# Kernel tuning notes

Measured on AMD Instinct MI355X. Metric: run time of the kernel, lower is better.

The kernel has to match this reference:

```python
import jax, jax.numpy as jnp
import numpy as np

N_NODES = 100000
N_EDGES = 1600000


def gcn_conv(h_in, row, col, W, b, num_nodes):
    """PyG-style GCNConv: linear transform, add self-loops, symmetric
    deg^{-1/2} normalization, scatter-add aggregation at target nodes."""
    h = h_in @ W  # [N, out]
    loops = jnp.arange(num_nodes, dtype=row.dtype)
    r = jnp.concatenate([row, loops])  # source
    c = jnp.concatenate([col, loops])  # target
    ew = jnp.ones(r.shape[0], dtype=h.dtype)
    deg = jax.ops.segment_sum(ew, c, num_segments=num_nodes)  # in-degree incl. self-loop
    dinv = jnp.where(deg > 0, jax.lax.rsqrt(deg), 0.0)
    norm = dinv[r] * dinv[c]  # [E+N]
    msgs = norm[:, None] * h[r]  # gather + scale, [E+N, out]
    out = jax.ops.segment_sum(msgs, c, num_segments=num_nodes)  # scatter-add
    return out + b


def setup_inputs() -> dict:
    key = jax.random.key(0)
    ks = jax.random.split(key, 8)
    in_f, hid, out_f = 128, 128, 64
    x = jax.random.normal(ks[0], (N_NODES, in_f), dtype=jnp.float32)
    edge_index = jax.random.randint(ks[1], (2, N_EDGES), 0, N_NODES, dtype=jnp.int64)
    edge_weight = jax.random.uniform(ks[2], (N_EDGES,), dtype=jnp.float32)
    s1 = 1.0 / np.sqrt(in_f)
    s2 = 1.0 / np.sqrt(hid)
    s3 = 1.0 / np.sqrt(out_f)
    W1 = jax.random.normal(ks[3], (in_f, hid), dtype=jnp.float32) * s1
    b1 = jnp.zeros((hid,), dtype=jnp.float32)
    W2 = jax.random.normal(ks[4], (hid, out_f), dtype=jnp.float32) * s2
    b2 = jnp.zeros((out_f,), dtype=jnp.float32)
    Wfc = jax.random.normal(ks[5], (out_f, 1), dtype=jnp.float32) * s3
    bfc = jnp.zeros((1,), dtype=jnp.float32)
    return {"x": x, "edge_index": edge_index, "edge_weight": edge_weight,
            "W1": W1, "b1": b1, "W2": W2, "b2": b2, "Wfc": Wfc, "bfc": bfc}


def reference(x, edge_index, edge_weight, W1, b1, W2, b2, Wfc, bfc):
    # eval mode: dropout(p=0.6) is identity; edge_weight is unused by the
    # original forward (edge_attr never passed to GCNConv).
    row, col = edge_index[0], edge_index[1]
    n = x.shape[0]
    h = jax.nn.relu(gcn_conv(x, row, col, W1, b1, n))
    h = gcn_conv(h, row, col, W2, b2, n)
    return h @ Wfc + bfc  # [N, 1]
```

## Files before the change

### kernel.cpp

```cpp
#include <hip/hip_runtime.h>
#include <cstddef>

#define CAP 64
#define BK_SHIFT 8
#define BSTRIDE 8192
#define CHUNK 2048

typedef unsigned int uint32;
typedef unsigned short ushort;
typedef __attribute__((ext_vector_type(8))) short short8;
typedef __attribute__((ext_vector_type(4))) float f32x4;
typedef __attribute__((ext_vector_type(4))) int int4v;
typedef __attribute__((ext_vector_type(4))) float float4v;

__device__ __forceinline__ float bf_lo(uint32 v) {
  union { uint32 u; float f; } c; c.u = v << 16; return c.f;
}
__device__ __forceinline__ float bf_hi(uint32 v) {
  union { uint32 u; float f; } c; c.u = v & 0xffff0000u; return c.f;
}
__device__ __forceinline__ uint32 pack_bf2(float a, float b) {
  union { float f; uint32 u; } x, y; x.f = a; y.f = b;
  uint32 ua = x.u + 0x7fffu + ((x.u >> 16) & 1u);
  uint32 ub = y.u + 0x7fffu + ((y.u >> 16) & 1u);
  return (ua >> 16) | (ub & 0xffff0000u);
}
__device__ __forceinline__ ushort bf16_1(float x) {
  union { float f; uint32 u; } c; c.f = x;
  return (ushort)((c.u + 0x7fffu + ((c.u >> 16) & 1u)) >> 16);
}

union ABu { uint32 u[4]; short8 v; };

__global__ __launch_bounds__(256) void k_part1(const int* __restrict__ ei,
                                               int* __restrict__ bcnt,
                                               int* __restrict__ stage,
                                               int E, int N, int NB) {
  __shared__ int hist[512];
  __shared__ int gbase[512];
  const int tid = threadIdx.x;
  const int base = blockIdx.x * CHUNK;
  for (int b = tid; b < NB; b += 256) hist[b] = 0;
  __syncthreads();
  int rr[8], cc[8], lp[8];
  #pragma unroll
  for (int j = 0; j < 8; j++) {
    int e = base + tid + j * 256;
    int r = -1, c = -1;
    if (e < E) {
      r = __builtin_nontemporal_load(&ei[e]);
      c = __builtin_nontemporal_load(&ei[(size_t)E + e]);
    }
    bool ok = ((unsigned)r < (unsigned)N) && ((unsigned)c < (unsigned)N);
    rr[j] = ok ? r : -1;
    cc[j] = c;
    lp[j] = ok ? atomicAdd(&hist[c >> BK_SHIFT], 1) : 0;
  }
  __syncthreads();
  for (int b = tid; b < NB; b += 256) {
    int h = hist[b];
    gbase[b] = h ? atomicAdd(&bcnt[b], h) : 0;
  }
  __syncthreads();
  #pragma unroll
  for (int j = 0; j < 8; j++) {
    if (rr[j] >= 0) {
      int b = cc[j] >> BK_SHIFT;
      int pos = gbase[b] + lp[j];
      if (pos < BSTRIDE)
        stage[(size_t)b * BSTRIDE + pos] = (rr[j] << 8) | (cc[j] & 255);
    }
  }
}

__global__ __launch_bounds__(256) void k_fill2(const int* __restrict__ stage,
                                               const int* __restrict__ bcnt,
                                               int* __restrict__ csr,
                                               int* __restrict__ cnt,
                                               float* __restrict__ dinv, int N, int NB,
                                               const float* __restrict__ W2,
                                               const float* __restrict__ Wfc,
                                               const float* __restrict__ b2,
                                               const float* __restrict__ bfc,
                                               float* __restrict__ wvo,
                                               float* __restrict__ c0) {
  const int b = blockIdx.x;
  const int tid = threadIdx.x;
  if (b == NB) {
    if (tid < 128) {
      float s = 0.f;
      #pragma unroll 8
      for (int j = 0; j < 64; j++) s += W2[tid * 64 + j] * Wfc[j];
      wvo[tid] = s;
      if (tid == 0) {
        float cc = 0.f;
        for (int j = 0; j < 64; j++) cc += b2[j] * Wfc[j];
        c0[0] = cc + bfc[0];
      }
    }
    return;
  }
  __shared__ int lc[256];
  lc[tid] = 0;
  __syncthreads();
  int m = bcnt[b]; if (m > BSTRIDE) m = BSTRIDE;
  const int node0 = b << BK_SHIFT;
  const int* __restrict__ sb = stage + (size_t)b * BSTRIDE;
  for (int e = tid; e < m; e += 256) {
    int v = __builtin_nontemporal_load(&sb[e]);
    int cl = v & 255;
    int r = v >> 8;
    int pos = atomicAdd(&lc[cl], 1);
    if (pos < CAP) csr[(size_t)(node0 + cl) * CAP + pos] = r;
  }
  __syncthreads();
  int node = node0 + tid;
  if (node < N) {
    int d = lc[tid]; if (d > CAP) d = CAP;
    cnt[node] = d;
    int d8 = (d + 7) & ~7; if (d8 > CAP) d8 = CAP;
    for (int p = d; p < d8; p++) csr[(size_t)node * CAP + p] = node;
    dinv[node] = rsqrtf((float)(lc[tid] + 1));
  }
}

__global__ __launch_bounds__(256) void k_gemm(const float* __restrict__ X,
                                              const float* __restrict__ W,
                                              const float* __restrict__ dinv,
                                              ushort* __restrict__ Xh, int M) {
  __shared__ ushort WtT[16384];
  const int tid  = threadIdx.x;
  const int lane = tid & 63;
  const int wv   = tid >> 6;
  const int cl   = lane & 15;
  const int g    = lane >> 4;

  const int rb = blockIdx.x * 64 + wv * 16;

  int rowc = rb + cl; if (rowc >= M) rowc = M - 1;
  const float* xr = X + (size_t)rowc * 128;
  ABu af[4];
  #pragma unroll
  for (int kk = 0; kk < 4; kk++) {
    float4v p = __builtin_nontemporal_load((const float4v*)&xr[kk * 32 + g * 8]);
    float4v q = __builtin_nontemporal_load((const float4v*)&xr[kk * 32 + g * 8 + 4]);
    af[kk].u[0] = pack_bf2(p.x, p.y);
    af[kk].u[1] = pack_bf2(p.z, p.w);
    af[kk].u[2] = pack_bf2(q.x, q.y);
    af[kk].u[3] = pack_bf2(q.z, q.w);
  }

  float dvr[4];
  #pragma unroll
  for (int r = 0; r < 4; r++) {
    int rw = rb + g * 4 + r; if (rw >= M) rw = M - 1;
    dvr[r] = dinv[rw];
  }

  for (int idx = tid; idx < 8192; idx += 256) {
    int k = idx >> 6;
    int c = (idx & 63) * 2;
    float2 w2 = *(const float2*)&W[k * 128 + c];
    int gr = ((k >> 3) ^ ((c & 15) >> 1)) & 15;
    int base = (gr << 4) + (k & 7) * 2;
    *(ushort*)((char*)WtT + c * 256 + base)       = bf16_1(w2.x);
    *(ushort*)((char*)WtT + (c + 1) * 256 + base) = bf16_1(w2.y);
  }
  __syncthreads();

  #pragma unroll
  for (int ct = 0; ct < 8; ct++) {
    const char* wrow = (const char*)WtT + (ct * 16 + cl) * 256;
    f32x4 acc = {0.f, 0.f, 0.f, 0.f};
    #pragma unroll
    for (int kk = 0; kk < 4; kk++) {
      int grn = ((4 * kk + g) ^ (cl >> 1)) & 15;
      short8 bfrag = *(const short8*)(wrow + (grn << 4));
      acc = __builtin_amdgcn_mfma_f32_16x16x32_bf16(af[kk].v, bfrag, acc, 0, 0, 0);
    }
    #pragma unroll
    for (int r = 0; r < 4; r++) {
      int rw = rb + g * 4 + r;
      if (rw < M) Xh[(size_t)rw * 128 + ct * 16 + cl] = bf16_1(dvr[r] * acc[r]);
    }
  }
}

__global__ __launch_bounds__(256) void k_agg1(const uint32* __restrict__ Xh,
                                              const int* __restrict__ csr,
                                              const int* __restrict__ cnt,
                                              const float* __restrict__ dinv,
                                              const float* __restrict__ b1,
                                              const float* __restrict__ wv,
                                              float* __restrict__ dz, int N) {
  int wid = (blockIdx.x * 256 + threadIdx.x) >> 6;
  int lane = threadIdx.x & 63;
  if (wid >= N) return;
  const int i = wid;
  int deg = cnt[i]; if (deg > CAP) deg = CAP;
  const int deg8 = (deg + 7) & ~7;
  const float di = dinv[i];
  int edge_reg = i;
  if (lane < deg8) edge_reg = __builtin_nontemporal_load(&csr[(size_t)i * CAP + lane]);

  uint32 vs = Xh[(size_t)i * 64 + lane];
  float a0x = 0.f, a0y = 0.f, a1x = 0.f, a1y = 0.f;
  float a2x = 0.f, a2y = 0.f, a3x = 0.f, a3y = 0.f;
  float a4x = 0.f, a4y = 0.f, a5x = 0.f, a5y = 0.f;
  float a6x = 0.f, a6y = 0.f, a7x = 0.f, a7y = 0.f;

  for (int e = 0; e < deg8; e += 8) {
    int s0 = __builtin_amdgcn_readlane(edge_reg, e + 0);
    int s1 = __builtin_amdgcn_readlane(edge_reg, e + 1);
    int s2 = __builtin_amdgcn_readlane(edge_reg, e + 2);
    int s3 = __builtin_amdgcn_readlane(edge_reg, e + 3);
    int s4 = __builtin_amdgcn_readlane(edge_reg, e + 4);
    int s5 = __builtin_amdgcn_readlane(edge_reg, e + 5);
    int s6 = __builtin_amdgcn_readlane(edge_reg, e + 6);
    int s7 = __builtin_amdgcn_readlane(edge_reg, e + 7);
    uint32 v0 = Xh[(size_t)s0 * 64 + lane];
    uint32 v1 = Xh[(size_t)s1 * 64 + lane];
    uint32 v2 = Xh[(size_t)s2 * 64 + lane];
    uint32 v3 = Xh[(size_t)s3 * 64 + lane];
    uint32 v4 = Xh[(size_t)s4 * 64 + lane];
    uint32 v5 = Xh[(size_t)s5 * 64 + lane];
    uint32 v6 = Xh[(size_t)s6 * 64 + lane];
    uint32 v7 = Xh[(size_t)s7 * 64 + lane];
    a0x += bf_lo(v0); a0y += bf_hi(v0);
    a1x += bf_lo(v1); a1y += bf_hi(v1);
    a2x += bf_lo(v2); a2y += bf_hi(v2);
    a3x += bf_lo(v3); a3y += bf_hi(v3);
    a4x += bf_lo(v4); a4y += bf_hi(v4);
    a5x += bf_lo(v5); a5y += bf_hi(v5);
    a6x += bf_lo(v6); a6y += bf_hi(v6);
    a7x += bf_lo(v7); a7y += bf_hi(v7);
  }
  const float selfc = 1.0f - (float)(deg8 - deg);
  float sx = ((a0x + a1x) + (a2x + a3x)) + ((a4x + a5x) + (a6x + a7x));
  float sy = ((a0y + a1y) + (a2y + a3y)) + ((a4y + a5y) + (a6y + a7y));
  sx = fmaf(selfc, bf_lo(vs), sx);
  sy = fmaf(selfc, bf_hi(vs), sy);

  float2 bb = *(const float2*)&b1[lane * 2];
  float h0 = fmaxf(fmaf(di, sx, bb.x), 0.f);
  float h1 = fmaxf(fmaf(di, sy, bb.y), 0.f);
  float2 ww = *(const float2*)&wv[lane * 2];
  float part = fmaf(h0, ww.x, h1 * ww.y);
  #pragma unroll
  for (int m = 32; m > 0; m >>= 1) part += __shfl_xor(part, m, 64);
  if (lane == 0) dz[i] = di * part;
}

__global__ __launch_bounds__(256) void k_out(const float* __restrict__ dz,
                                             const int* __restrict__ csr,
                                             const int* __restrict__ cnt,
                                             const float* __restrict__ dinv,
                                             const float* __restrict__ c0,
                                             float* __restrict__ out, int N) {
  int i = blockIdx.x * 256 + threadIdx.x;
  if (i >= N) return;
  int deg = cnt[i]; if (deg > CAP) deg = CAP;
  const int deg8 = (deg + 7) & ~7;
  const int4v* __restrict__ edges = (const int4v*)(csr + (size_t)i * CAP);
  float s0 = (1.0f - (float)(deg8 - deg)) * dz[i];
  float s1 = 0.f, s2 = 0.f, s3 = 0.f;
  for (int e4 = 0; e4 < (deg8 >> 2); e4 += 2) {
    int4v q0 = __builtin_nontemporal_load(&edges[e4]);
    int4v q1 = __builtin_nontemporal_load(&edges[e4 + 1]);
    s0 += dz[q0.x]; s1 += dz[q0.y]; s2 += dz[q0.z]; s3 += dz[q0.w];
    s0 += dz[q1.x]; s1 += dz[q1.y]; s2 += dz[q1.z]; s3 += dz[q1.w];
  }
  out[i] = dinv[i] * ((s0 + s1) + (s2 + s3)) + c0[0];
}

extern "C" void kernel_launch(void* const* d_in, const int* in_sizes, int n_in,
                              void* d_out, int out_size, void* d_ws, size_t ws_size,
                              hipStream_t stream) {
  const float* x   = (const float*)d_in[0];
  const int*   ei  = (const int*)d_in[1];
  const float* W1  = (const float*)d_in[3];
  const float* b1  = (const float*)d_in[4];
  const float* W2  = (const float*)d_in[5];
  const float* b2  = (const float*)d_in[6];
  const float* Wfc = (const float*)d_in[7];
  const float* bfc = (const float*)d_in[8];
  float* out = (float*)d_out;

  const int N = in_sizes[0] / 128;
  const int E = in_sizes[1] / 2;
  const int NB = (N + 255) >> 8;

  char* ws = (char*)d_ws;
  ushort* Xh  = (ushort*)(ws);
  int*   stage= (int*)   (ws);
  int*   csr  = (int*)   (ws + (size_t)N * 256);
  int*   cnt  = (int*)   (ws + (size_t)N * 512);
  float* dinv = (float*) (ws + (size_t)N * 516);
  float* dz   = (float*) (ws + (size_t)N * 520);
  int*   bcnt = (int*)dz;
  float* wv   = (float*) (ws + (size_t)N * 524);
  float* c0   = wv + 128;

  hipMemsetAsync(bcnt, 0, (size_t)NB * 4, stream);
  hipLaunchKernelGGL(k_part1, dim3((E + CHUNK - 1) / CHUNK), dim3(256), 0, stream,
                     ei, bcnt, stage, E, N, NB);
  hipLaunchKernelGGL(k_fill2, dim3(NB + 1), dim3(256), 0, stream,
                     stage, bcnt, csr, cnt, dinv, N, NB, W2, Wfc, b2, bfc, wv, c0);
  hipLaunchKernelGGL(k_gemm,  dim3((N + 63) / 64), dim3(256), 0, stream,
                     x, W1, dinv, Xh, N);
  hipLaunchKernelGGL(k_agg1,  dim3(((size_t)N * 64 + 255) / 256), dim3(256), 0, stream,
                     (const uint32*)Xh, csr, cnt, dinv, b1, wv, dz, N);
  hipLaunchKernelGGL(k_out,   dim3((N + 255) / 256), dim3(256), 0, stream,
                     dz, csr, cnt, dinv, c0, out, N);
}
```

Baseline: 161.9 us.

## Slice hidden features into 16-wide planes and aggregate per slice with reduction

The GEMM output is stored as eight feature-sliced planes of 16 bf16 values per node. The first aggregation is rewritten so that each wave handles eight nodes, with eight lanes per node gathering 32-byte rows from a single slice. Partial dot products go to a per-slice buffer, and a new reduction kernel sums them into dz. The stored dinv array is dropped and rsqrt is recomputed from the degree counts, which adds a launch and extra partial-sum traffic in exchange for narrower, more parallel gathers.

```diff
diff --git a/kernel.cpp b/kernel.cpp
--- a/kernel.cpp
+++ b/kernel.cpp
@@ -76,8 +76,7 @@
 __global__ __launch_bounds__(256) void k_fill2(const int* __restrict__ stage,
                                                const int* __restrict__ bcnt,
                                                int* __restrict__ csr,
-                                               int* __restrict__ cnt,
-                                               float* __restrict__ dinv, int N, int NB,
+                                               int* __restrict__ cnt, int N, int NB,
                                                const float* __restrict__ W2,
                                                const float* __restrict__ Wfc,
                                                const float* __restrict__ b2,
@@ -120,22 +119,21 @@
     cnt[node] = d;
     int d8 = (d + 7) & ~7; if (d8 > CAP) d8 = CAP;
     for (int p = d; p < d8; p++) csr[(size_t)node * CAP + p] = node;
-    dinv[node] = rsqrtf((float)(lc[tid] + 1));
   }
 }
 
 __global__ __launch_bounds__(256) void k_gemm(const float* __restrict__ X,
                                               const float* __restrict__ W,
-                                              const float* __restrict__ dinv,
-                                              ushort* __restrict__ Xh, int M) {
+                                              const int* __restrict__ cnt,
+                                              ushort* __restrict__ Xh8, int M) {
   __shared__ ushort WtT[16384];
   const int tid  = threadIdx.x;
   const int lane = tid & 63;
   const int wv   = tid >> 6;
   const int cl   = lane & 15;
   const int g    = lane >> 4;
-
   const int rb = blockIdx.x * 64 + wv * 16;
+  const size_t SL = (size_t)M * 16;
 
   int rowc = rb + cl; if (rowc >= M) rowc = M - 1;
   const float* xr = X + (size_t)rowc * 128;
@@ -154,7 +152,7 @@
   #pragma unroll
   for (int r = 0; r < 4; r++) {
     int rw = rb + g * 4 + r; if (rw >= M) rw = M - 1;
-    dvr[r] = dinv[rw];
+    dvr[r] = rsqrtf((float)(cnt[rw] + 1));
   }
 
   for (int idx = tid; idx < 8192; idx += 256) {
@@ -181,80 +179,69 @@
     #pragma unroll
     for (int r = 0; r < 4; r++) {
       int rw = rb + g * 4 + r;
-      if (rw < M) Xh[(size_t)rw * 128 + ct * 16 + cl] = bf16_1(dvr[r] * acc[r]);
-    }
-  }
-}
-
-__global__ __launch_bounds__(256) void k_agg1(const uint32* __restrict__ Xh,
-                                              const int* __restrict__ csr,
-                                              const int* __restrict__ cnt,
-                                              const float* __restrict__ dinv,
-                                              const float* __restrict__ b1,
-                                              const float* __restrict__ wv,
-                                              float* __restrict__ dz, int N) {
-  int wid = (blockIdx.x * 256 + threadIdx.x) >> 6;
-  int lane = threadIdx.x & 63;
-  if (wid >= N) return;
-  const int i = wid;
+      if (rw < M) Xh8[(size_t)ct * SL + (size_t)rw * 16 + cl] = bf16_1(dvr[r] * acc[r]);
+    }
+  }
+}
+
+__global__ __launch_bounds__(256) void k_agg1s(const ushort* __restrict__ Xh8,
+                                               const int* __restrict__ csr,
+                                               const int* __restrict__ cnt,
+                                               const float* __restrict__ b1,
+                                               const float* __restrict__ wvv,
+                                               float* __restrict__ dzp, int M, int N) {
+  const int tid  = threadIdx.x;
+  const int s    = blockIdx.x & 7;
+  const int chnk = blockIdx.x >> 3;
+  const int lane = tid & 63;
+  const int ld   = lane & 7;
+  const int i    = chnk * 32 + (tid >> 6) * 8 + (lane >> 3);
+  if (i >= N) return;
+  const uint32* __restrict__ Xs = (const uint32*)(Xh8 + (size_t)s * (size_t)M * 16);
+
   int deg = cnt[i]; if (deg > CAP) deg = CAP;
   const int deg8 = (deg + 7) & ~7;
-  const float di = dinv[i];
-  int edge_reg = i;
-  if (lane < deg8) edge_reg = __builtin_nontemporal_load(&csr[(size_t)i * CAP + lane]);
-
-  uint32 vs = Xh[(size_t)i * 64 + lane];
-  float a0x = 0.f, a0y = 0.f, a1x = 0.f, a1y = 0.f;
-  float a2x = 0.f, a2y = 0.f, a3x = 0.f, a3y = 0.f;
-  float a4x = 0.f, a4y = 0.f, a5x = 0.f, a5y = 0.f;
-  float a6x = 0.f, a6y = 0.f, a7x = 0.f, a7y = 0.f;
-
-  for (int e = 0; e < deg8; e += 8) {
-    int s0 = __builtin_amdgcn_readlane(edge_reg, e + 0);
-    int s1 = __builtin_amdgcn_readlane(edge_reg, e + 1);
-    int s2 = __builtin_amdgcn_readlane(edge_reg, e + 2);
-    int s3 = __builtin_amdgcn_readlane(edge_reg, e + 3);
-    int s4 = __builtin_amdgcn_readlane(edge_reg, e + 4);
-    int s5 = __builtin_amdgcn_readlane(edge_reg, e + 5);
-    int s6 = __builtin_amdgcn_readlane(edge_reg, e + 6);
-    int s7 = __builtin_amdgcn_readlane(edge_reg, e + 7);
-    uint32 v0 = Xh[(size_t)s0 * 64 + lane];
-    uint32 v1 = Xh[(size_t)s1 * 64 + lane];
-    uint32 v2 = Xh[(size_t)s2 * 64 + lane];
-    uint32 v3 = Xh[(size_t)s3 * 64 + lane];
-    uint32 v4 = Xh[(size_t)s4 * 64 + lane];
-    uint32 v5 = Xh[(size_t)s5 * 64 + lane];
-    uint32 v6 = Xh[(size_t)s6 * 64 + lane];
-    uint32 v7 = Xh[(size_t)s7 * 64 + lane];
-    a0x += bf_lo(v0); a0y += bf_hi(v0);
-    a1x += bf_lo(v1); a1y += bf_hi(v1);
-    a2x += bf_lo(v2); a2y += bf_hi(v2);
-    a3x += bf_lo(v3); a3y += bf_hi(v3);
-    a4x += bf_lo(v4); a4y += bf_hi(v4);
-    a5x += bf_lo(v5); a5y += bf_hi(v5);
-    a6x += bf_lo(v6); a6y += bf_hi(v6);
-    a7x += bf_lo(v7); a7y += bf_hi(v7);
-  }
+  const float di = rsqrtf((float)(deg + 1));
+
+  float ax = 0.f, ay = 0.f;
+  for (int base = 0; base < deg8; base += 8) {
+    int ereg = __builtin_nontemporal_load(&csr[(size_t)i * CAP + base + ld]);
+    #pragma unroll
+    for (int j = 0; j < 8; j++) {
+      int src = __shfl(ereg, (lane & 56) + j, 64);
+      uint32 u = Xs[(size_t)src * 8 + ld];
+      ax += bf_lo(u); ay += bf_hi(u);
+    }
+  }
+  uint32 su = Xs[(size_t)i * 8 + ld];
   const float selfc = 1.0f - (float)(deg8 - deg);
-  float sx = ((a0x + a1x) + (a2x + a3x)) + ((a4x + a5x) + (a6x + a7x));
-  float sy = ((a0y + a1y) + (a2y + a3y)) + ((a4y + a5y) + (a6y + a7y));
-  sx = fmaf(selfc, bf_lo(vs), sx);
-  sy = fmaf(selfc, bf_hi(vs), sy);
-
-  float2 bb = *(const float2*)&b1[lane * 2];
-  float h0 = fmaxf(fmaf(di, sx, bb.x), 0.f);
-  float h1 = fmaxf(fmaf(di, sy, bb.y), 0.f);
-  float2 ww = *(const float2*)&wv[lane * 2];
-  float part = fmaf(h0, ww.x, h1 * ww.y);
-  #pragma unroll
-  for (int m = 32; m > 0; m >>= 1) part += __shfl_xor(part, m, 64);
-  if (lane == 0) dz[i] = di * part;
+  ax = fmaf(selfc, bf_lo(su), ax);
+  ay = fmaf(selfc, bf_hi(su), ay);
+
+  int f = s * 16 + 2 * ld;
+  float h0 = fmaxf(fmaf(di, ax, b1[f]), 0.f);
+  float h1 = fmaxf(fmaf(di, ay, b1[f + 1]), 0.f);
+  float part = fmaf(h0, wvv[f], h1 * wvv[f + 1]);
+  part += __shfl_xor(part, 1, 64);
+  part += __shfl_xor(part, 2, 64);
+  part += __shfl_xor(part, 4, 64);
+  if (ld == 0) dzp[(size_t)s * N + i] = part;
+}
+
+__global__ __launch_bounds__(256) void k_red(const float* __restrict__ dzp,
+                                             const int* __restrict__ cnt,
+                                             float* __restrict__ dz, int N) {
+  int i = blockIdx.x * 256 + threadIdx.x;
+  if (i >= N) return;
+  float s = 0.f;
+  #pragma unroll
+  for (int k = 0; k < 8; k++) s += dzp[(size_t)k * N + i];
+  dz[i] = rsqrtf((float)(cnt[i] + 1)) * s;
 }
 
 __global__ __launch_bounds__(256) void k_out(const float* __restrict__ dz,
                                              const int* __restrict__ csr,
                                              const int* __restrict__ cnt,
-                                             const float* __restrict__ dinv,
                                              const float* __restrict__ c0,
                                              float* __restrict__ out, int N) {
   int i = blockIdx.x * 256 + threadIdx.x;
@@ -270,7 +257,7 @@
     s0 += dz[q0.x]; s1 += dz[q0.y]; s2 += dz[q0.z]; s3 += dz[q0.w];
     s0 += dz[q1.x]; s1 += dz[q1.y]; s2 += dz[q1.z]; s3 += dz[q1.w];
   }
-  out[i] = dinv[i] * ((s0 + s1) + (s2 + s3)) + c0[0];
+  out[i] = rsqrtf((float)(cnt[i] + 1)) * ((s0 + s1) + (s2 + s3)) + c0[0];
 }
 
 extern "C" void kernel_launch(void* const* d_in, const int* in_sizes, int n_in,
@@ -291,25 +278,29 @@
   const int NB = (N + 255) >> 8;
 
   char* ws = (char*)d_ws;
-  ushort* Xh  = (ushort*)(ws);
-  int*   stage= (int*)   (ws);
-  int*   csr  = (int*)   (ws + (size_t)N * 256);
-  int*   cnt  = (int*)   (ws + (size_t)N * 512);
-  float* dinv = (float*) (ws + (size_t)N * 516);
-  float* dz   = (float*) (ws + (size_t)N * 520);
-  int*   bcnt = (int*)dz;
-  float* wv   = (float*) (ws + (size_t)N * 524);
-  float* c0   = wv + 128;
+  ushort* Xh8 = (ushort*)(ws);
+  size_t off = (size_t)N * 256;
+  int* csr   = (int*)(ws + off); off += (size_t)N * 256;
+  int* stage = (int*)(ws + off);
+  float* dzp = (float*)stage;
+  off += (size_t)NB * BSTRIDE * 4;
+  int* cnt   = (int*)(ws + off); off += (size_t)N * 4;
+  float* dz  = (float*)(ws + off); off += (size_t)N * 4;
+  int* bcnt  = (int*)(ws + off); off += (size_t)NB * 4;
+  float* wv  = (float*)(ws + off); off += 512;
+  float* c0  = (float*)(ws + off);
 
   hipMemsetAsync(bcnt, 0, (size_t)NB * 4, stream);
   hipLaunchKernelGGL(k_part1, dim3((E + CHUNK - 1) / CHUNK), dim3(256), 0, stream,
                      ei, bcnt, stage, E, N, NB);
   hipLaunchKernelGGL(k_fill2, dim3(NB + 1), dim3(256), 0, stream,
-                     stage, bcnt, csr, cnt, dinv, N, NB, W2, Wfc, b2, bfc, wv, c0);
+                     stage, bcnt, csr, cnt, N, NB, W2, Wfc, b2, bfc, wv, c0);
   hipLaunchKernelGGL(k_gemm,  dim3((N + 63) / 64), dim3(256), 0, stream,
-                     x, W1, dinv, Xh, N);
-  hipLaunchKernelGGL(k_agg1,  dim3(((size_t)N * 64 + 255) / 256), dim3(256), 0, stream,
-                     (const uint32*)Xh, csr, cnt, dinv, b1, wv, dz, N);
+                     x, W1, cnt, Xh8, N);
+  hipLaunchKernelGGL(k_agg1s, dim3(((N + 31) / 32) * 8), dim3(256), 0, stream,
+                     Xh8, csr, cnt, b1, wv, dzp, N, N);
+  hipLaunchKernelGGL(k_red,   dim3((N + 255) / 256), dim3(256), 0, stream,
+                     dzp, cnt, dz, N);
   hipLaunchKernelGGL(k_out,   dim3((N + 255) / 256), dim3(256), 0, stream,
-                     dz, csr, cnt, dinv, c0, out, N);
-}
+                     dz, csr, cnt, c0, out, N);
+}
```

Result: slower. 222.1 us (+37.2%).

## Count degrees in partition pass and fuse CSR fill with GEMM launch

Applied to the files above, without the earlier changes.

Node in-degrees are now counted with global atomics during the edge-partition pass. The degree normalisation can then be recomputed from the counts on the fly, and the dinv array goes away. That lets the CSR fill blocks and the first-layer GEMM blocks share a single launch, so the two independent stages overlap and one launch boundary disappears. Edge and stage loads are also widened to int4 vectors. In exchange, 1.6M scattered global atomics are added, and the workspace grows because stage no longer aliases Xh.

```diff
diff --git a/kernel.cpp b/kernel.cpp
--- a/kernel.cpp
+++ b/kernel.cpp
@@ -35,6 +35,7 @@
 __global__ __launch_bounds__(256) void k_part1(const int* __restrict__ ei,
                                                int* __restrict__ bcnt,
                                                int* __restrict__ stage,
+                                               int* __restrict__ cnt,
                                                int E, int N, int NB) {
   __shared__ int hist[512];
   __shared__ int gbase[512];
@@ -44,17 +45,28 @@
   __syncthreads();
   int rr[8], cc[8], lp[8];
   #pragma unroll
-  for (int j = 0; j < 8; j++) {
-    int e = base + tid + j * 256;
-    int r = -1, c = -1;
-    if (e < E) {
-      r = __builtin_nontemporal_load(&ei[e]);
-      c = __builtin_nontemporal_load(&ei[(size_t)E + e]);
-    }
-    bool ok = ((unsigned)r < (unsigned)N) && ((unsigned)c < (unsigned)N);
-    rr[j] = ok ? r : -1;
-    cc[j] = c;
-    lp[j] = ok ? atomicAdd(&hist[c >> BK_SHIFT], 1) : 0;
+  for (int h = 0; h < 2; h++) {
+    int e0 = base + h * 1024 + tid * 4;
+    int4v r4 = {-1, -1, -1, -1}, c4 = {-1, -1, -1, -1};
+    if (e0 + 3 < E) {
+      r4 = __builtin_nontemporal_load((const int4v*)&ei[e0]);
+      c4 = __builtin_nontemporal_load((const int4v*)&ei[(size_t)E + e0]);
+    } else {
+      for (int j = 0; j < 4; j++)
+        if (e0 + j < E) {
+          ((int*)&r4)[j] = ei[e0 + j];
+          ((int*)&c4)[j] = ei[(size_t)E + e0 + j];
+        }
+    }
+    #pragma unroll
+    for (int j = 0; j < 4; j++) {
+      int r = ((int*)&r4)[j], c = ((int*)&c4)[j];
+      bool ok = ((unsigned)r < (unsigned)N) && ((unsigned)c < (unsigned)N);
+      rr[h * 4 + j] = ok ? r : -1;
+      cc[h * 4 + j] = c;
+      lp[h * 4 + j] = ok ? atomicAdd(&hist[c >> BK_SHIFT], 1) : 0;
+      if (ok) atomicAdd(&cnt[c], 1);
+    }
   }
   __syncthreads();
   for (int b = tid; b < NB; b += 256) {
@@ -73,20 +85,67 @@
   }
 }
 
-__global__ __launch_bounds__(256) void k_fill2(const int* __restrict__ stage,
+__global__ __launch_bounds__(256) void k_build(const int* __restrict__ stage,
                                                const int* __restrict__ bcnt,
                                                int* __restrict__ csr,
-                                               int* __restrict__ cnt,
-                                               float* __restrict__ dinv, int N, int NB,
+                                               const int* __restrict__ cnt,
+                                               const float* __restrict__ X,
+                                               const float* __restrict__ W,
+                                               ushort* __restrict__ Xh,
+                                               int M, int NB, int ngemm,
                                                const float* __restrict__ W2,
                                                const float* __restrict__ Wfc,
                                                const float* __restrict__ b2,
                                                const float* __restrict__ bfc,
                                                float* __restrict__ wvo,
                                                float* __restrict__ c0) {
-  const int b = blockIdx.x;
+  __shared__ ushort WtT[16384];
+  __shared__ int lc[256];
   const int tid = threadIdx.x;
-  if (b == NB) {
+  const int bx  = blockIdx.x;
+
+  if (bx < NB) {
+    lc[tid] = 0;
+    __syncthreads();
+    int m = bcnt[bx]; if (m > BSTRIDE) m = BSTRIDE;
+    const int node0 = bx << BK_SHIFT;
+    const int* __restrict__ sb = stage + (size_t)bx * BSTRIDE;
+    int e = tid * 4;
+    for (; e + 3 < m; e += 1024) {
+      int4v v4 = __builtin_nontemporal_load((const int4v*)&sb[e]);
+      #pragma unroll
+      for (int j = 0; j < 4; j++) {
+        int v = ((int*)&v4)[j];
+        int pos = atomicAdd(&lc[v & 255], 1);
+        if (pos < CAP) csr[(size_t)(node0 + (v & 255)) * CAP + pos] = v >> 8;
+      }
+    }
+    for (int ee = e; ee < m; ee++) {
+      if ((ee & 3) == 0 || ee == e) {}
+      int v = sb[ee];
+      (void)v;
+      break;
+    }
+    if (tid == 255) {
+      int mt = m & ~3;
+      int estart = mt;
+      for (int ee = estart; ee < m; ee++) {
+        int v = sb[ee];
+        int pos = atomicAdd(&lc[v & 255], 1);
+        if (pos < CAP) csr[(size_t)(node0 + (v & 255)) * CAP + pos] = v >> 8;
+      }
+    }
+    __syncthreads();
+    int node = node0 + tid;
+    if (node < M) {
+      int d = lc[tid]; if (d > CAP) d = CAP;
+      int d8 = (d + 7) & ~7; if (d8 > CAP) d8 = CAP;
+      for (int p = d; p < d8; p++) csr[(size_t)node * CAP + p] = node;
+    }
+    return;
+  }
+
+  if (bx == NB + ngemm) {
     if (tid < 128) {
       float s = 0.f;
       #pragma unroll 8
@@ -100,42 +159,12 @@
     }
     return;
   }
-  __shared__ int lc[256];
-  lc[tid] = 0;
-  __syncthreads();
-  int m = bcnt[b]; if (m > BSTRIDE) m = BSTRIDE;
-  const int node0 = b << BK_SHIFT;
-  const int* __restrict__ sb = stage + (size_t)b * BSTRIDE;
-  for (int e = tid; e < m; e += 256) {
-    int v = __builtin_nontemporal_load(&sb[e]);
-    int cl = v & 255;
-    int r = v >> 8;
-    int pos = atomicAdd(&lc[cl], 1);
-    if (pos < CAP) csr[(size_t)(node0 + cl) * CAP + pos] = r;
-  }
-  __syncthreads();
-  int node = node0 + tid;
-  if (node < N) {
-    int d = lc[tid]; if (d > CAP) d = CAP;
-    cnt[node] = d;
-    int d8 = (d + 7) & ~7; if (d8 > CAP) d8 = CAP;
-    for (int p = d; p < d8; p++) csr[(size_t)node * CAP + p] = node;
-    dinv[node] = rsqrtf((float)(lc[tid] + 1));
-  }
-}
-
-__global__ __launch_bounds__(256) void k_gemm(const float* __restrict__ X,
-                                              const float* __restrict__ W,
-                                              const float* __restrict__ dinv,
-                                              ushort* __restrict__ Xh, int M) {
-  __shared__ ushort WtT[16384];
-  const int tid  = threadIdx.x;
+
   const int lane = tid & 63;
   const int wv   = tid >> 6;
   const int cl   = lane & 15;
   const int g    = lane >> 4;
-
-  const int rb = blockIdx.x * 64 + wv * 16;
+  const int rb = (bx - NB) * 64 + wv * 16;
 
   int rowc = rb + cl; if (rowc >= M) rowc = M - 1;
   const float* xr = X + (size_t)rowc * 128;
@@ -154,7 +183,7 @@
   #pragma unroll
   for (int r = 0; r < 4; r++) {
     int rw = rb + g * 4 + r; if (rw >= M) rw = M - 1;
-    dvr[r] = dinv[rw];
+    dvr[r] = rsqrtf((float)(cnt[rw] + 1));
   }
 
   for (int idx = tid; idx < 8192; idx += 256) {
@@ -189,7 +218,6 @@
 __global__ __launch_bounds__(256) void k_agg1(const uint32* __restrict__ Xh,
                                               const int* __restrict__ csr,
                                               const int* __restrict__ cnt,
-                                              const float* __restrict__ dinv,
                                               const float* __restrict__ b1,
                                               const float* __restrict__ wv,
                                               float* __restrict__ dz, int N) {
@@ -197,9 +225,10 @@
   int lane = threadIdx.x & 63;
   if (wid >= N) return;
   const int i = wid;
-  int deg = cnt[i]; if (deg > CAP) deg = CAP;
+  int cv = cnt[i];
+  int deg = cv; if (deg > CAP) deg = CAP;
   const int deg8 = (deg + 7) & ~7;
-  const float di = dinv[i];
+  const float di = rsqrtf((float)(cv + 1));
   int edge_reg = i;
   if (lane < deg8) edge_reg = __builtin_nontemporal_load(&csr[(size_t)i * CAP + lane]);
 
@@ -254,12 +283,12 @@
 __global__ __launch_bounds__(256) void k_out(const float* __restrict__ dz,
                                              const int* __restrict__ csr,
                                              const int* __restrict__ cnt,
-                                             const float* __restrict__ dinv,
                                              const float* __restrict__ c0,
                                              float* __restrict__ out, int N) {
   int i = blockIdx.x * 256 + threadIdx.x;
   if (i >= N) return;
-  int deg = cnt[i]; if (deg > CAP) deg = CAP;
+  int cv = cnt[i];
+  int deg = cv; if (deg > CAP) deg = CAP;
   const int deg8 = (deg + 7) & ~7;
   const int4v* __restrict__ edges = (const int4v*)(csr + (size_t)i * CAP);
   float s0 = (1.0f - (float)(deg8 - deg)) * dz[i];
@@ -270,7 +299,7 @@
     s0 += dz[q0.x]; s1 += dz[q0.y]; s2 += dz[q0.z]; s3 += dz[q0.w];
     s0 += dz[q1.x]; s1 += dz[q1.y]; s2 += dz[q1.z]; s3 += dz[q1.w];
   }
-  out[i] = dinv[i] * ((s0 + s1) + (s2 + s3)) + c0[0];
+  out[i] = rsqrtf((float)(cv + 1)) * ((s0 + s1) + (s2 + s3)) + c0[0];
 }
 
 extern "C" void kernel_launch(void* const* d_in, const int* in_sizes, int n_in,
@@ -291,25 +320,25 @@
   const int NB = (N + 255) >> 8;
 
   char* ws = (char*)d_ws;
-  ushort* Xh  = (ushort*)(ws);
-  int*   stage= (int*)   (ws);
-  int*   csr  = (int*)   (ws + (size_t)N * 256);
-  int*   cnt  = (int*)   (ws + (size_t)N * 512);
-  float* dinv = (float*) (ws + (size_t)N * 516);
-  float* dz   = (float*) (ws + (size_t)N * 520);
-  int*   bcnt = (int*)dz;
-  float* wv   = (float*) (ws + (size_t)N * 524);
-  float* c0   = wv + 128;
-
-  hipMemsetAsync(bcnt, 0, (size_t)NB * 4, stream);
+  ushort* Xh = (ushort*)(ws);
+  size_t off = (size_t)N * 256;
+  int* csr   = (int*)(ws + off); off += (size_t)N * 256;
+  int* stage = (int*)(ws + off); off += (size_t)NB * BSTRIDE * 4;
+  int* cnt   = (int*)(ws + off); off += (size_t)N * 4;
+  int* bcnt  = (int*)(ws + off); off += (size_t)NB * 4;
+  float* dz  = (float*)(ws + off); off += (size_t)N * 4;
+  float* wv  = (float*)(ws + off); off += 512;
+  float* c0  = (float*)(ws + off);
+
+  hipMemsetAsync(cnt, 0, (size_t)(N + NB) * 4, stream);
   hipLaunchKernelGGL(k_part1, dim3((E + CHUNK - 1) / CHUNK), dim3(256), 0, stream,
-                     ei, bcnt, stage, E, N, NB);
-  hipLaunchKernelGGL(k_fill2, dim3(NB + 1), dim3(256), 0, stream,
-                     stage, bcnt, csr, cnt, dinv, N, NB, W2, Wfc, b2, bfc, wv, c0);
-  hipLaunchKernelGGL(k_gemm,  dim3((N + 63) / 64), dim3(256), 0, stream,
-                     x, W1, dinv, Xh, N);
-  hipLaunchKernelGGL(k_agg1,  dim3(((size_t)N * 64 + 255) / 256), dim3(256), 0, stream,
-                     (const uint32*)Xh, csr, cnt, dinv, b1, wv, dz, N);
-  hipLaunchKernelGGL(k_out,   dim3((N + 255) / 256), dim3(256), 0, stream,
-                     dz, csr, cnt, dinv, c0, out, N);
-}
+                     ei, bcnt, stage, cnt, E, N, NB);
+  const int ngemm = (N + 63) / 64;
+  hipLaunchKernelGGL(k_build, dim3(NB + ngemm + 1), dim3(256), 0, stream,
+                     stage, bcnt, csr, cnt, x, W1, Xh, N, NB, ngemm,
+                     W2, Wfc, b2, bfc, wv, c0);
+  hipLaunchKernelGGL(k_agg1, dim3(((size_t)N * 64 + 255) / 256), dim3(256), 0, stream,
+                     (const uint32*)Xh, csr, cnt, b1, wv, dz, N);
+  hipLaunchKernelGGL(k_out,  dim3((N + 255) / 256), dim3(256), 0, stream,
+                     dz, csr, cnt, c0, out, N);
+}
```

Result: slower. 209.0 us (+29.1%).
